# Kernel tuning notes

Hardware: AMD Instinct MI355X
Metric: run time of the kernel (lower is better)

Reference implementation:

```python
import jax, jax.numpy as jnp
import numpy as np

N_NODES = 100000
N_EDGES = 1600000
N_GRAPHS = 512
HIDDEN = 128
N_LAYERS = 3


def setup_inputs() -> dict:
    key = jax.random.key(0)
    ks = jax.random.split(key, 16)
    X = jax.random.normal(ks[0], (N_NODES, HIDDEN), dtype=jnp.float32)
    edge_index = jax.random.randint(ks[1], (2, N_EDGES), 0, N_NODES, dtype=jnp.int64)
    batch = jnp.sort(jax.random.randint(ks[2], (N_NODES,), 0, N_GRAPHS, dtype=jnp.int64))
    s = 1.0 / np.sqrt(HIDDEN)
    mlp_w1 = jax.random.normal(ks[3], (N_LAYERS, HIDDEN, HIDDEN), dtype=jnp.float32) * s
    mlp_b1 = jnp.zeros((N_LAYERS, HIDDEN), dtype=jnp.float32)
    mlp_w2 = jax.random.normal(ks[4], (N_LAYERS, HIDDEN, HIDDEN), dtype=jnp.float32) * s
    mlp_b2 = jnp.zeros((N_LAYERS, HIDDEN), dtype=jnp.float32)
    cls_w1 = jax.random.normal(ks[5], (HIDDEN * N_LAYERS, HIDDEN), dtype=jnp.float32) / np.sqrt(HIDDEN * N_LAYERS)
    cls_b1 = jnp.zeros((HIDDEN,), dtype=jnp.float32)
    cls_w2 = jax.random.normal(ks[6], (HIDDEN, HIDDEN), dtype=jnp.float32) * s
    cls_b2 = jnp.zeros((HIDDEN,), dtype=jnp.float32)
    cls_w3 = jax.random.normal(ks[7], (HIDDEN, 1), dtype=jnp.float32) * s
    cls_b3 = jnp.zeros((1,), dtype=jnp.float32)
    return {"X": X, "edge_index": edge_index, "batch": batch,
            "mlp_w1": mlp_w1, "mlp_b1": mlp_b1, "mlp_w2": mlp_w2, "mlp_b2": mlp_b2,
            "cls_w1": cls_w1, "cls_b1": cls_b1, "cls_w2": cls_w2, "cls_b2": cls_b2,
            "cls_w3": cls_w3, "cls_b3": cls_b3}


def reference(X, edge_index, batch, mlp_w1, mlp_b1, mlp_w2, mlp_b2,
              cls_w1, cls_b1, cls_w2, cls_b2, cls_w3, cls_b3):
    src, dst = edge_index[0], edge_index[1]
    xs = []
    for l in range(N_LAYERS):
        # GIN aggregation: sum_{j in N(i)} x_j ; eps = 0 so add self feature
        agg = jax.ops.segment_sum(X[src], dst, num_segments=N_NODES)  # [N, H]
        z = X + agg
        # 2-layer MLP update
        h = jax.nn.relu(z @ mlp_w1[l] + mlp_b1[l])
        h = h @ mlp_w2[l] + mlp_b2[l]
        # dropout is identity in eval; then relu
        X = jax.nn.relu(h)
        # global sum pooling per graph
        xs.append(jax.ops.segment_sum(X, batch, num_segments=N_GRAPHS))  # [G, H]
    h = jnp.concatenate(xs, axis=-1)  # JK 'cat' -> [G, H*L]
    h = jax.nn.relu(h @ cls_w1 + cls_b1)
    h = jax.nn.relu(h @ cls_w2 + cls_b2)
    logits = h @ cls_w3 + cls_b3  # [G, 1]
    return logits
```

## Files before the change

kernel.cpp:

```cpp
#include <hip/hip_runtime.h>
#include <hip/hip_fp16.h>
#include <cstddef>
#include <cstdint>

#define N_NODES   100000
#define N_EDGES   1600000
#define N_GRAPHS  512
#define HIDDEN    128
#define N_LAYERS  3

#define N_WIN        400
#define WIN_NODES    (N_NODES / N_WIN)
#define PLACE_BLOCKS 128
#define PCHUNK       (N_EDGES / PLACE_BLOCKS)

typedef _Float16 half8  __attribute__((ext_vector_type(8)));
typedef _Float16 half2v __attribute__((ext_vector_type(2)));
typedef float    float8 __attribute__((ext_vector_type(8)));
typedef float    floatx4 __attribute__((ext_vector_type(4)));
typedef float    floatx2 __attribute__((ext_vector_type(2)));

__global__ __launch_bounds__(256) void win_count_kernel(const int* __restrict__ dst,
                                                        int* __restrict__ counts) {
    __shared__ int cs[N_WIN];
    for (int i = threadIdx.x; i < N_WIN; i += 256) cs[i] = 0;
    __syncthreads();
    const int4* d4 = (const int4*)(dst + blockIdx.x * PCHUNK);
    for (int i = threadIdx.x; i < PCHUNK / 4; i += 256) {
        int4 d = d4[i];
        atomicAdd(&cs[d.x / WIN_NODES], 1);
        atomicAdd(&cs[d.y / WIN_NODES], 1);
        atomicAdd(&cs[d.z / WIN_NODES], 1);
        atomicAdd(&cs[d.w / WIN_NODES], 1);
    }
    __syncthreads();
    for (int i = threadIdx.x; i < N_WIN; i += 256)
        counts[blockIdx.x * N_WIN + i] = cs[i];
}

__global__ __launch_bounds__(128) void win_scan1_kernel(const int* __restrict__ counts,
                                                        int* __restrict__ offsets,
                                                        int* __restrict__ colsum) {
    __shared__ int tmp[128];
    const int w = blockIdx.x;
    const int t = threadIdx.x;
    tmp[t] = counts[t * N_WIN + w];
    __syncthreads();
#pragma unroll
    for (int off = 1; off < 128; off <<= 1) {
        int u = (t >= off) ? tmp[t - off] : 0;
        __syncthreads();
        tmp[t] += u;
        __syncthreads();
    }
    offsets[t * N_WIN + w] = (t == 0) ? 0 : tmp[t - 1];
    if (t == 127) colsum[w] = tmp[127];
}

__global__ __launch_bounds__(512) void win_scan2_kernel(const int* __restrict__ colsum,
                                                        int* __restrict__ winbase) {
    __shared__ int tmp[512];
    const int t = threadIdx.x;
    tmp[t] = (t < N_WIN) ? colsum[t] : 0;
    __syncthreads();
#pragma unroll
    for (int off = 1; off < 512; off <<= 1) {
        int u = (t >= off) ? tmp[t - off] : 0;
        __syncthreads();
        tmp[t] += u;
        __syncthreads();
    }
    if (t < N_WIN) winbase[t] = (t == 0) ? 0 : tmp[t - 1];
    if (t == N_WIN - 1) winbase[N_WIN] = tmp[t];
}

__global__ __launch_bounds__(256) void win_place_kernel(const int* __restrict__ src,
                                                        const int* __restrict__ dst,
                                                        const int* __restrict__ offsets,
                                                        const int* __restrict__ winbase,
                                                        int2* __restrict__ wedge) {
    __shared__ int off[N_WIN];
    for (int i = threadIdx.x; i < N_WIN; i += 256)
        off[i] = offsets[blockIdx.x * N_WIN + i] + winbase[i];
    __syncthreads();
    const int4* d4 = (const int4*)(dst + blockIdx.x * PCHUNK);
    const int4* s4 = (const int4*)(src + blockIdx.x * PCHUNK);
    for (int i = threadIdx.x; i < PCHUNK / 4; i += 256) {
        int4 d = d4[i];
        int4 s = s4[i];
        int p0 = atomicAdd(&off[d.x / WIN_NODES], 1); wedge[p0] = make_int2(d.x, s.x);
        int p1 = atomicAdd(&off[d.y / WIN_NODES], 1); wedge[p1] = make_int2(d.y, s.y);
        int p2 = atomicAdd(&off[d.z / WIN_NODES], 1); wedge[p2] = make_int2(d.z, s.z);
        int p3 = atomicAdd(&off[d.w / WIN_NODES], 1); wedge[p3] = make_int2(d.w, s.w);
    }
}

__global__ __launch_bounds__(256) void win_csr_kernel(const int2* __restrict__ wedge,
                                                      const int* __restrict__ winbase,
                                                      int* __restrict__ row_ptr,
                                                      int* __restrict__ csr_src) {
    __shared__ int cnt[WIN_NODES];
    __shared__ int tmp[256];
    const int w = blockIdx.x, n0 = w * WIN_NODES, t = threadIdx.x;
    for (int i = t; i < WIN_NODES; i += 256) cnt[i] = 0;
    __syncthreads();
    const int b0 = winbase[w], b1 = winbase[w + 1];
    for (int e = b0 + t; e < b1; e += 256)
        atomicAdd(&cnt[wedge[e].x - n0], 1);
    __syncthreads();
    tmp[t] = (t < WIN_NODES) ? cnt[t] : 0;
    __syncthreads();
#pragma unroll
    for (int off = 1; off < 256; off <<= 1) {
        int u = (t >= off) ? tmp[t - off] : 0;
        __syncthreads();
        tmp[t] += u;
        __syncthreads();
    }
    const int excl = (t == 0) ? 0 : tmp[t - 1];
    if (t < WIN_NODES) {
        row_ptr[n0 + t] = b0 + excl;
        cnt[t] = b0 + excl;
    }
    if (w == N_WIN - 1 && t == 0) row_ptr[N_NODES] = winbase[N_WIN];
    __syncthreads();
    for (int e = b0 + t; e < b1; e += 256) {
        int2 ed = wedge[e];
        int p = atomicAdd(&cnt[ed.x - n0], 1);
        csr_src[p] = ed.y;
    }
}

__global__ void f2h_kernel(const float* __restrict__ in, __half* __restrict__ out,
                           unsigned char* __restrict__ outq) {
    int t = blockIdx.x * blockDim.x + threadIdx.x;
    const int n8 = (N_NODES * HIDDEN) / 8;
    if (t >= n8) return;
    const float4* in4 = (const float4*)in;
    float4 a = in4[t * 2 + 0];
    float4 b = in4[t * 2 + 1];
    __half2* o2 = (__half2*)out;
    o2[t * 4 + 0] = __floats2half2_rn(a.x, a.y);
    o2[t * 4 + 1] = __floats2half2_rn(a.z, a.w);
    o2[t * 4 + 2] = __floats2half2_rn(b.x, b.y);
    o2[t * 4 + 3] = __floats2half2_rn(b.z, b.w);
    unsigned r0 = 0, r1 = 0;
    r0 = __builtin_amdgcn_cvt_pk_fp8_f32(a.x, a.y, r0, false);
    r0 = __builtin_amdgcn_cvt_pk_fp8_f32(a.z, a.w, r0, true);
    r1 = __builtin_amdgcn_cvt_pk_fp8_f32(b.x, b.y, r1, false);
    r1 = __builtin_amdgcn_cvt_pk_fp8_f32(b.z, b.w, r1, true);
    ((uint2*)outq)[t] = make_uint2(r0, r1);
}

__global__ __launch_bounds__(256) void wconv_kernel(const float* __restrict__ w1,
                                                    const float* __restrict__ w2,
                                                    __half* __restrict__ wt1,
                                                    __half* __restrict__ wt2) {
    __shared__ float tile[32][33];
    const int b = blockIdx.x;
    const int mat = b & 1;
    const int tt = (b >> 1) & 15;
    const int l  = b >> 5;
    const int ti = (tt >> 2) * 32, tj = (tt & 3) * 32;
    const float* W = (mat ? w2 : w1) + (size_t)l * HIDDEN * HIDDEN;
    __half* WT = (mat ? wt2 : wt1) + (size_t)l * HIDDEN * HIDDEN;
    const int r = threadIdx.x >> 5;
    const int c = threadIdx.x & 31;
#pragma unroll
    for (int rr = 0; rr < 4; ++rr)
        tile[r + 8 * rr][c] = W[(size_t)(ti + r + 8 * rr) * HIDDEN + tj + c];
    __syncthreads();
#pragma unroll
    for (int rr = 0; rr < 4; ++rr)
        WT[(size_t)(tj + r + 8 * rr) * HIDDEN + ti + c] =
            __float2half(tile[c][r + 8 * rr]);
}

__device__ __forceinline__ void acc_fp8x16(float* acc, uint4 v) {
    floatx2 f;
    f = __builtin_amdgcn_cvt_pk_f32_fp8(v.x, false); acc[0] += f.x;  acc[1] += f.y;
    f = __builtin_amdgcn_cvt_pk_f32_fp8(v.x, true);  acc[2] += f.x;  acc[3] += f.y;
    f = __builtin_amdgcn_cvt_pk_f32_fp8(v.y, false); acc[4] += f.x;  acc[5] += f.y;
    f = __builtin_amdgcn_cvt_pk_f32_fp8(v.y, true);  acc[6] += f.x;  acc[7] += f.y;
    f = __builtin_amdgcn_cvt_pk_f32_fp8(v.z, false); acc[8] += f.x;  acc[9] += f.y;
    f = __builtin_amdgcn_cvt_pk_f32_fp8(v.z, true);  acc[10] += f.x; acc[11] += f.y;
    f = __builtin_amdgcn_cvt_pk_f32_fp8(v.w, false); acc[12] += f.x; acc[13] += f.y;
    f = __builtin_amdgcn_cvt_pk_f32_fp8(v.w, true);  acc[14] += f.x; acc[15] += f.y;
}

__global__ void gather_kernel(const unsigned char* __restrict__ Xq,
                              const __half* __restrict__ Xh,
                              __half* __restrict__ Zh,
                              const int* __restrict__ row_ptr,
                              const int* __restrict__ csr_src) {
    int wave = (blockIdx.x * blockDim.x + threadIdx.x) >> 6;
    int lane = threadIdx.x & 63;
    if (wave >= N_NODES) return;
    const int grp = lane >> 3;
    const int m   = lane & 7;
    const uint4* Q = (const uint4*)Xq;

    float acc[16];
#pragma unroll
    for (int j = 0; j < 16; ++j) acc[j] = 0.f;

    int k = row_ptr[wave];
    const int end = row_ptr[wave + 1];

    for (; k + 16 <= end; k += 16) {
        int n0 = csr_src[k + grp];
        int n1 = csr_src[k + 8 + grp];
        uint4 v0 = Q[(size_t)n0 * 8 + m];
        uint4 v1 = Q[(size_t)n1 * 8 + m];
        acc_fp8x16(acc, v0);
        acc_fp8x16(acc, v1);
    }
    if (k + 8 <= end) {
        int n0 = csr_src[k + grp];
        uint4 v0 = Q[(size_t)n0 * 8 + m];
        acc_fp8x16(acc, v0);
        k += 8;
    }
    int rem = end - k;
    if (grp < rem) {
        int n0 = csr_src[k + grp];
        uint4 v0 = Q[(size_t)n0 * 8 + m];
        acc_fp8x16(acc, v0);
    }

    half2v hh[8];
#pragma unroll
    for (int j = 0; j < 8; ++j) {
        hh[j][0] = (_Float16)acc[2 * j];
        hh[j][1] = (_Float16)acc[2 * j + 1];
    }
#pragma unroll
    for (int j = 0; j < 8; ++j) {
        int b = __shfl_xor(__builtin_bit_cast(int, hh[j]), 8);
        hh[j] = hh[j] + __builtin_bit_cast(half2v, b);
    }
#pragma unroll
    for (int j = 0; j < 8; ++j) {
        int b = __shfl_xor(__builtin_bit_cast(int, hh[j]), 16);
        hh[j] = hh[j] + __builtin_bit_cast(half2v, b);
    }
#pragma unroll
    for (int j = 0; j < 8; ++j) {
        int b = __shfl_xor(__builtin_bit_cast(int, hh[j]), 32);
        hh[j] = hh[j] + __builtin_bit_cast(half2v, b);
    }

    if (grp == 0) {
        const half2v* H2 = (const half2v*)(Xh + (size_t)wave * HIDDEN + 16 * m);
        half8 o0, o1;
#pragma unroll
        for (int j = 0; j < 4; ++j) {
            half2v s = hh[j] + H2[j];
            o0[2 * j] = s[0]; o0[2 * j + 1] = s[1];
        }
#pragma unroll
        for (int j = 0; j < 4; ++j) {
            half2v s = hh[4 + j] + H2[4 + j];
            o1[2 * j] = s[0]; o1[2 * j + 1] = s[1];
        }
        ((half8*)(Zh + (size_t)wave * HIDDEN + 16 * m))[0] = o0;
        ((half8*)(Zh + (size_t)wave * HIDDEN + 16 * m))[1] = o1;
    }
}

#define MM_BLOCKS 512
__global__ __launch_bounds__(256, 2) void mm_stage_kernel(const __half* __restrict__ A,
                                                          const __half* __restrict__ Wt,
                                                          const float* __restrict__ bias,
                                                          __half* __restrict__ C16) {
    const int gwave = (blockIdx.x * 256 + threadIdx.x) >> 6;
    const int lane  = threadIdx.x & 63;
    const int m = lane & 15;
    const int q = lane >> 4;
    const int nwaves = MM_BLOCKS * 4;
    const int NTILES = N_NODES / 16;

    half8 wf[8][4];
    float bl[8];
#pragma unroll
    for (int ct = 0; ct < 8; ++ct) {
        const half8* Wrow = (const half8*)(Wt + (size_t)(ct * 16 + m) * HIDDEN);
#pragma unroll
        for (int c = 0; c < 4; ++c) wf[ct][c] = Wrow[c * 4 + q];
        bl[ct] = bias[ct * 16 + m];
    }

    for (int t = gwave; t < NTILES; t += nwaves) {
        const half8* Arow = (const half8*)(A + (size_t)(t * 16 + m) * HIDDEN);
        half8 a0 = Arow[q];
        half8 a1 = Arow[4 + q];
        half8 a2 = Arow[8 + q];
        half8 a3 = Arow[12 + q];
#pragma unroll
        for (int ct = 0; ct < 8; ++ct) {
            floatx4 acc = {0.f, 0.f, 0.f, 0.f};
            acc = __builtin_amdgcn_mfma_f32_16x16x32_f16(a0, wf[ct][0], acc, 0, 0, 0);
            acc = __builtin_amdgcn_mfma_f32_16x16x32_f16(a1, wf[ct][1], acc, 0, 0, 0);
            acc = __builtin_amdgcn_mfma_f32_16x16x32_f16(a2, wf[ct][2], acc, 0, 0, 0);
            acc = __builtin_amdgcn_mfma_f32_16x16x32_f16(a3, wf[ct][3], acc, 0, 0, 0);
            const int n = ct * 16 + m;
#pragma unroll
            for (int r = 0; r < 4; ++r) {
                int row = t * 16 + q * 4 + r;
                float v = fmaxf(acc[r] + bl[ct], 0.f);
                C16[(size_t)row * HIDDEN + n] = __float2half(v);
            }
        }
    }
}

#define POOL_CHUNK 32
__global__ __launch_bounds__(64) void pool_kernel(const __half* __restrict__ Xh,
                                                  const int* __restrict__ batch,
                                                  float* __restrict__ pooled, int layer,
                                                  unsigned char* __restrict__ outq) {
    const int f2 = threadIdx.x;
    int start = blockIdx.x * POOL_CHUNK;
    int end = start + POOL_CHUNK;
    if (end > N_NODES) end = N_NODES;
    float ax = 0.f, ay = 0.f;
    int gcur = batch[start];
    for (int n = start; n < end; ++n) {
        int g = batch[n];
        if (g != gcur) {
            float* pd = &pooled[(size_t)gcur * (HIDDEN * N_LAYERS) + layer * HIDDEN + 2 * f2];
            atomicAdd(pd, ax);
            atomicAdd(pd + 1, ay);
            ax = 0.f; ay = 0.f;
            gcur = g;
        }
        __half2 v = ((const __half2*)(Xh + (size_t)n * HIDDEN))[f2];
        float2 fv = __half22float2(v);
        ax += fv.x; ay += fv.y;
        if (outq) {
            unsigned r = __builtin_amdgcn_cvt_pk_fp8_f32(fv.x, fv.y, 0, false);
            ((unsigned short*)(outq + (size_t)n * HIDDEN))[f2] = (unsigned short)(r & 0xffff);
        }
    }
    float* pd = &pooled[(size_t)gcur * (HIDDEN * N_LAYERS) + layer * HIDDEN + 2 * f2];
    atomicAdd(pd, ax);
    atomicAdd(pd + 1, ay);
}

__global__ __launch_bounds__(128) void cls_kernel(const float* __restrict__ pooled,
                                                  const float* __restrict__ w1,
                                                  const float* __restrict__ b1,
                                                  const float* __restrict__ w2,
                                                  const float* __restrict__ b2,
                                                  const float* __restrict__ w3,
                                                  const float* __restrict__ b3,
                                                  float* __restrict__ out) {
    __shared__ float hin[HIDDEN * N_LAYERS];
    __shared__ float h1[HIDDEN];
    __shared__ float red[HIDDEN];
    const int g = blockIdx.x;
    const int t = threadIdx.x;

    for (int i = t; i < HIDDEN * N_LAYERS; i += 128)
        hin[i] = pooled[(size_t)g * (HIDDEN * N_LAYERS) + i];
    __syncthreads();

    float s = 0.f;
    for (int k = 0; k < HIDDEN * N_LAYERS; ++k) s += hin[k] * w1[(size_t)k * HIDDEN + t];
    s = fmaxf(s + b1[t], 0.f);
    h1[t] = s;
    __syncthreads();

    float s2 = 0.f;
    for (int k = 0; k < HIDDEN; ++k) s2 += h1[k] * w2[(size_t)k * HIDDEN + t];
    s2 = fmaxf(s2 + b2[t], 0.f);

    red[t] = s2 * w3[t];
    __syncthreads();
    for (int off = 64; off > 0; off >>= 1) {
        if (t < off) red[t] += red[t + off];
        __syncthreads();
    }
    if (t == 0) out[g] = red[0] + b3[0];
}

extern "C" void kernel_launch(void* const* d_in, const int* in_sizes, int n_in,
                              void* d_out, int out_size, void* d_ws, size_t ws_size,
                              hipStream_t stream) {
    const float* X     = (const float*)d_in[0];
    const int*   ei    = (const int*)d_in[1];
    const int*   batch = (const int*)d_in[2];
    const float* w1all = (const float*)d_in[3];
    const float* b1all = (const float*)d_in[4];
    const float* w2all = (const float*)d_in[5];
    const float* b2all = (const float*)d_in[6];
    const float* cw1   = (const float*)d_in[7];
    const float* cb1   = (const float*)d_in[8];
    const float* cw2   = (const float*)d_in[9];
    const float* cb2   = (const float*)d_in[10];
    const float* cw3   = (const float*)d_in[11];
    const float* cb3   = (const float*)d_in[12];
    float* out = (float*)d_out;

    const int* src = ei;
    const int* dst = ei + N_EDGES;

    char* p = (char*)d_ws;
    auto alloc2 = [&](size_t bytes) {
        char* r = p;
        p += (bytes + 255) & ~(size_t)255;
        return r;
    };
    __half* hA      = (__half*)alloc2((size_t)N_NODES * HIDDEN * sizeof(__half));
    __half* hB      = (__half*)alloc2((size_t)N_NODES * HIDDEN * sizeof(__half));
    __half* zh      = (__half*)alloc2((size_t)N_NODES * HIDDEN * sizeof(__half));
    __half* m1h     = (__half*)alloc2((size_t)N_NODES * HIDDEN * sizeof(__half));
    unsigned char* qbuf = (unsigned char*)alloc2((size_t)N_NODES * HIDDEN);
    __half* wt1     = (__half*)alloc2((size_t)N_LAYERS * HIDDEN * HIDDEN * sizeof(__half));
    __half* wt2     = (__half*)alloc2((size_t)N_LAYERS * HIDDEN * HIDDEN * sizeof(__half));
    int2*   wedge   = (int2*)alloc2((size_t)N_EDGES * sizeof(int2));
    int*    csr     = (int*)alloc2((size_t)N_EDGES * sizeof(int));
    int*    rowp    = (int*)alloc2((size_t)(N_NODES + 1) * sizeof(int));
    int*    counts  = (int*)alloc2((size_t)PLACE_BLOCKS * N_WIN * sizeof(int));
    int*    offsets = (int*)alloc2((size_t)PLACE_BLOCKS * N_WIN * sizeof(int));
    int*    colsum  = (int*)alloc2((size_t)N_WIN * sizeof(int));
    int*    winbase = (int*)alloc2((size_t)(N_WIN + 1) * sizeof(int));
    float*  pooled  = (float*)alloc2((size_t)N_GRAPHS * HIDDEN * N_LAYERS * sizeof(float));

    hipMemsetAsync(pooled, 0, (size_t)N_GRAPHS * HIDDEN * N_LAYERS * sizeof(float), stream);

    win_count_kernel<<<PLACE_BLOCKS, 256, 0, stream>>>(dst, counts);
    win_scan1_kernel<<<N_WIN, 128, 0, stream>>>(counts, offsets, colsum);
    win_scan2_kernel<<<1, 512, 0, stream>>>(colsum, winbase);
    win_place_kernel<<<PLACE_BLOCKS, 256, 0, stream>>>(src, dst, offsets, winbase, wedge);
    win_csr_kernel<<<N_WIN, 256, 0, stream>>>(wedge, winbase, rowp, csr);

    const int cvt_grid = ((N_NODES * HIDDEN / 8) + 255) / 256;
    f2h_kernel<<<cvt_grid, 256, 0, stream>>>(X, hA, qbuf);
    wconv_kernel<<<N_LAYERS * 2 * 16, 256, 0, stream>>>(w1all, w2all, wt1, wt2);

    const int gat_grid  = (N_NODES + 3) / 4;
    const int pool_grid = (N_NODES + POOL_CHUNK - 1) / POOL_CHUNK;

    __half* hcur = hA;
    for (int l = 0; l < N_LAYERS; ++l) {
        __half* hnext = (l & 1) ? hA : hB;
        gather_kernel<<<gat_grid, 256, 0, stream>>>(qbuf, hcur, zh, rowp, csr);
        mm_stage_kernel<<<MM_BLOCKS, 256, 0, stream>>>(zh,
                                                       wt1 + (size_t)l * HIDDEN * HIDDEN,
                                                       b1all + (size_t)l * HIDDEN,
                                                       m1h);
        mm_stage_kernel<<<MM_BLOCKS, 256, 0, stream>>>(m1h,
                                                       wt2 + (size_t)l * HIDDEN * HIDDEN,
                                                       b2all + (size_t)l * HIDDEN,
                                                       hnext);
        pool_kernel<<<pool_grid, 64, 0, stream>>>(hnext, batch, pooled, l,
                                                  (l < N_LAYERS - 1) ? qbuf : nullptr);
        hcur = hnext;
    }

    cls_kernel<<<N_GRAPHS, 128, 0, stream>>>(pooled, cw1, cb1, cw2, cb2, cw3, cb3, out);
}
```

Measured before the change: 487.5 us.

## Fuse setup kernels, inline window scan, and vectorize MFMA output stores

Removes the single-block window scan kernel by having each place and CSR block redundantly recompute the 400-entry prefix sum in shared memory. It also merges the fp16/fp8 input conversion, weight transpose and pooled-buffer zeroing into one prep kernel, which replaces a memset and two launches. Separately, the MLP matmul swaps its MFMA operands so each lane holds four consecutive output columns and writes them with one 8-byte store instead of four scattered 2-byte stores. The cost is redundant scan work in every block and larger 512-thread blocks for the graph-building kernels.

```diff
diff --git a/kernel.cpp b/kernel.cpp
--- a/kernel.cpp
+++ b/kernel.cpp
@@ -14,7 +14,13 @@
 #define PLACE_BLOCKS 128
 #define PCHUNK       (N_EDGES / PLACE_BLOCKS)
 
+#define F2H_BLOCKS   ((N_NODES * HIDDEN / 8) / 256)
+#define WCONV_BLOCKS (N_LAYERS * 2 * 16)
+#define PZERO_BLOCKS ((N_GRAPHS * HIDDEN * N_LAYERS) / 256)
+#define PREP_BLOCKS  (F2H_BLOCKS + WCONV_BLOCKS + PZERO_BLOCKS)
+
 typedef _Float16 half8  __attribute__((ext_vector_type(8)));
+typedef _Float16 half4v __attribute__((ext_vector_type(4)));
 typedef _Float16 half2v __attribute__((ext_vector_type(2)));
 typedef float    float8 __attribute__((ext_vector_type(8)));
 typedef float    floatx4 __attribute__((ext_vector_type(4)));
@@ -57,35 +63,28 @@
     if (t == 127) colsum[w] = tmp[127];
 }
 
-__global__ __launch_bounds__(512) void win_scan2_kernel(const int* __restrict__ colsum,
-                                                        int* __restrict__ winbase) {
-    __shared__ int tmp[512];
-    const int t = threadIdx.x;
-    tmp[t] = (t < N_WIN) ? colsum[t] : 0;
-    __syncthreads();
-#pragma unroll
-    for (int off = 1; off < 512; off <<= 1) {
-        int u = (t >= off) ? tmp[t - off] : 0;
-        __syncthreads();
-        tmp[t] += u;
-        __syncthreads();
-    }
-    if (t < N_WIN) winbase[t] = (t == 0) ? 0 : tmp[t - 1];
-    if (t == N_WIN - 1) winbase[N_WIN] = tmp[t];
-}
-
-__global__ __launch_bounds__(256) void win_place_kernel(const int* __restrict__ src,
+__global__ __launch_bounds__(512) void win_place_kernel(const int* __restrict__ src,
                                                         const int* __restrict__ dst,
                                                         const int* __restrict__ offsets,
-                                                        const int* __restrict__ winbase,
+                                                        const int* __restrict__ colsum,
                                                         int2* __restrict__ wedge) {
+    __shared__ int ws[512];
     __shared__ int off[N_WIN];
-    for (int i = threadIdx.x; i < N_WIN; i += 256)
-        off[i] = offsets[blockIdx.x * N_WIN + i] + winbase[i];
+    const int t = threadIdx.x;
+    ws[t] = (t < N_WIN) ? colsum[t] : 0;
+    __syncthreads();
+#pragma unroll
+    for (int o = 1; o < 512; o <<= 1) {
+        int u = (t >= o) ? ws[t - o] : 0;
+        __syncthreads();
+        ws[t] += u;
+        __syncthreads();
+    }
+    if (t < N_WIN) off[t] = offsets[blockIdx.x * N_WIN + t] + ((t == 0) ? 0 : ws[t - 1]);
     __syncthreads();
     const int4* d4 = (const int4*)(dst + blockIdx.x * PCHUNK);
     const int4* s4 = (const int4*)(src + blockIdx.x * PCHUNK);
-    for (int i = threadIdx.x; i < PCHUNK / 4; i += 256) {
+    for (int i = t; i < PCHUNK / 4; i += 512) {
         int4 d = d4[i];
         int4 s = s4[i];
         int p0 = atomicAdd(&off[d.x / WIN_NODES], 1); wedge[p0] = make_int2(d.x, s.x);
@@ -95,85 +94,101 @@
     }
 }
 
-__global__ __launch_bounds__(256) void win_csr_kernel(const int2* __restrict__ wedge,
-                                                      const int* __restrict__ winbase,
+__global__ __launch_bounds__(512) void win_csr_kernel(const int2* __restrict__ wedge,
+                                                      const int* __restrict__ colsum,
                                                       int* __restrict__ row_ptr,
                                                       int* __restrict__ csr_src) {
+    __shared__ int ws[512];
     __shared__ int cnt[WIN_NODES];
-    __shared__ int tmp[256];
+    __shared__ int bb[2];
     const int w = blockIdx.x, n0 = w * WIN_NODES, t = threadIdx.x;
-    for (int i = t; i < WIN_NODES; i += 256) cnt[i] = 0;
-    __syncthreads();
-    const int b0 = winbase[w], b1 = winbase[w + 1];
-    for (int e = b0 + t; e < b1; e += 256)
+    ws[t] = (t < N_WIN) ? colsum[t] : 0;
+    __syncthreads();
+#pragma unroll
+    for (int o = 1; o < 512; o <<= 1) {
+        int u = (t >= o) ? ws[t - o] : 0;
+        __syncthreads();
+        ws[t] += u;
+        __syncthreads();
+    }
+    if (t == 0) { bb[0] = (w > 0) ? ws[w - 1] : 0; bb[1] = ws[w]; }
+    if (w == N_WIN - 1 && t == 0) row_ptr[N_NODES] = ws[N_WIN - 1];
+    for (int i = t; i < WIN_NODES; i += 512) cnt[i] = 0;
+    __syncthreads();
+    const int b0 = bb[0], b1 = bb[1];
+    for (int e = b0 + t; e < b1; e += 512)
         atomicAdd(&cnt[wedge[e].x - n0], 1);
     __syncthreads();
-    tmp[t] = (t < WIN_NODES) ? cnt[t] : 0;
-    __syncthreads();
-#pragma unroll
-    for (int off = 1; off < 256; off <<= 1) {
-        int u = (t >= off) ? tmp[t - off] : 0;
-        __syncthreads();
-        tmp[t] += u;
-        __syncthreads();
-    }
-    const int excl = (t == 0) ? 0 : tmp[t - 1];
+    ws[t] = (t < WIN_NODES) ? cnt[t] : 0;
+    __syncthreads();
+#pragma unroll
+    for (int o = 1; o < 512; o <<= 1) {
+        int u = (t >= o) ? ws[t - o] : 0;
+        __syncthreads();
+        ws[t] += u;
+        __syncthreads();
+    }
+    const int excl = (t == 0) ? 0 : ws[t - 1];
     if (t < WIN_NODES) {
         row_ptr[n0 + t] = b0 + excl;
         cnt[t] = b0 + excl;
     }
-    if (w == N_WIN - 1 && t == 0) row_ptr[N_NODES] = winbase[N_WIN];
-    __syncthreads();
-    for (int e = b0 + t; e < b1; e += 256) {
+    __syncthreads();
+    for (int e = b0 + t; e < b1; e += 512) {
         int2 ed = wedge[e];
         int p = atomicAdd(&cnt[ed.x - n0], 1);
         csr_src[p] = ed.y;
     }
 }
 
-__global__ void f2h_kernel(const float* __restrict__ in, __half* __restrict__ out,
-                           unsigned char* __restrict__ outq) {
-    int t = blockIdx.x * blockDim.x + threadIdx.x;
-    const int n8 = (N_NODES * HIDDEN) / 8;
-    if (t >= n8) return;
-    const float4* in4 = (const float4*)in;
-    float4 a = in4[t * 2 + 0];
-    float4 b = in4[t * 2 + 1];
-    __half2* o2 = (__half2*)out;
-    o2[t * 4 + 0] = __floats2half2_rn(a.x, a.y);
-    o2[t * 4 + 1] = __floats2half2_rn(a.z, a.w);
-    o2[t * 4 + 2] = __floats2half2_rn(b.x, b.y);
-    o2[t * 4 + 3] = __floats2half2_rn(b.z, b.w);
-    unsigned r0 = 0, r1 = 0;
-    r0 = __builtin_amdgcn_cvt_pk_fp8_f32(a.x, a.y, r0, false);
-    r0 = __builtin_amdgcn_cvt_pk_fp8_f32(a.z, a.w, r0, true);
-    r1 = __builtin_amdgcn_cvt_pk_fp8_f32(b.x, b.y, r1, false);
-    r1 = __builtin_amdgcn_cvt_pk_fp8_f32(b.z, b.w, r1, true);
-    ((uint2*)outq)[t] = make_uint2(r0, r1);
-}
-
-__global__ __launch_bounds__(256) void wconv_kernel(const float* __restrict__ w1,
-                                                    const float* __restrict__ w2,
-                                                    __half* __restrict__ wt1,
-                                                    __half* __restrict__ wt2) {
+__global__ __launch_bounds__(256) void prep_kernel(const float* __restrict__ X,
+                                                   __half* __restrict__ hA,
+                                                   unsigned char* __restrict__ outq,
+                                                   const float* __restrict__ w1,
+                                                   const float* __restrict__ w2,
+                                                   __half* __restrict__ wt1,
+                                                   __half* __restrict__ wt2,
+                                                   float* __restrict__ pooled) {
     __shared__ float tile[32][33];
     const int b = blockIdx.x;
-    const int mat = b & 1;
-    const int tt = (b >> 1) & 15;
-    const int l  = b >> 5;
-    const int ti = (tt >> 2) * 32, tj = (tt & 3) * 32;
-    const float* W = (mat ? w2 : w1) + (size_t)l * HIDDEN * HIDDEN;
-    __half* WT = (mat ? wt2 : wt1) + (size_t)l * HIDDEN * HIDDEN;
-    const int r = threadIdx.x >> 5;
-    const int c = threadIdx.x & 31;
-#pragma unroll
-    for (int rr = 0; rr < 4; ++rr)
-        tile[r + 8 * rr][c] = W[(size_t)(ti + r + 8 * rr) * HIDDEN + tj + c];
-    __syncthreads();
-#pragma unroll
-    for (int rr = 0; rr < 4; ++rr)
-        WT[(size_t)(tj + r + 8 * rr) * HIDDEN + ti + c] =
-            __float2half(tile[c][r + 8 * rr]);
+    if (b < F2H_BLOCKS) {
+        int t = b * 256 + threadIdx.x;
+        const float4* in4 = (const float4*)X;
+        float4 a = in4[t * 2 + 0];
+        float4 c = in4[t * 2 + 1];
+        __half2* o2 = (__half2*)hA;
+        o2[t * 4 + 0] = __floats2half2_rn(a.x, a.y);
+        o2[t * 4 + 1] = __floats2half2_rn(a.z, a.w);
+        o2[t * 4 + 2] = __floats2half2_rn(c.x, c.y);
+        o2[t * 4 + 3] = __floats2half2_rn(c.z, c.w);
+        unsigned r0 = 0, r1 = 0;
+        r0 = __builtin_amdgcn_cvt_pk_fp8_f32(a.x, a.y, r0, false);
+        r0 = __builtin_amdgcn_cvt_pk_fp8_f32(a.z, a.w, r0, true);
+        r1 = __builtin_amdgcn_cvt_pk_fp8_f32(c.x, c.y, r1, false);
+        r1 = __builtin_amdgcn_cvt_pk_fp8_f32(c.z, c.w, r1, true);
+        ((uint2*)outq)[t] = make_uint2(r0, r1);
+    } else if (b < F2H_BLOCKS + WCONV_BLOCKS) {
+        const int bb = b - F2H_BLOCKS;
+        const int mat = bb & 1;
+        const int tt = (bb >> 1) & 15;
+        const int l  = bb >> 5;
+        const int ti = (tt >> 2) * 32, tj = (tt & 3) * 32;
+        const float* W = (mat ? w2 : w1) + (size_t)l * HIDDEN * HIDDEN;
+        __half* WT = (mat ? wt2 : wt1) + (size_t)l * HIDDEN * HIDDEN;
+        const int r = threadIdx.x >> 5;
+        const int c = threadIdx.x & 31;
+#pragma unroll
+        for (int rr = 0; rr < 4; ++rr)
+            tile[r + 8 * rr][c] = W[(size_t)(ti + r + 8 * rr) * HIDDEN + tj + c];
+        __syncthreads();
+#pragma unroll
+        for (int rr = 0; rr < 4; ++rr)
+            WT[(size_t)(tj + r + 8 * rr) * HIDDEN + ti + c] =
+                __float2half(tile[c][r + 8 * rr]);
+    } else {
+        int idx = (b - F2H_BLOCKS - WCONV_BLOCKS) * 256 + threadIdx.x;
+        pooled[idx] = 0.f;
+    }
 }
 
 __device__ __forceinline__ void acc_fp8x16(float* acc, uint4 v) {
@@ -281,13 +296,14 @@
     const int NTILES = N_NODES / 16;
 
     half8 wf[8][4];
-    float bl[8];
+    float bl[8][4];
 #pragma unroll
     for (int ct = 0; ct < 8; ++ct) {
         const half8* Wrow = (const half8*)(Wt + (size_t)(ct * 16 + m) * HIDDEN);
 #pragma unroll
         for (int c = 0; c < 4; ++c) wf[ct][c] = Wrow[c * 4 + q];
-        bl[ct] = bias[ct * 16 + m];
+#pragma unroll
+        for (int r = 0; r < 4; ++r) bl[ct][r] = bias[ct * 16 + q * 4 + r];
     }
 
     for (int t = gwave; t < NTILES; t += nwaves) {
@@ -296,20 +312,19 @@
         half8 a1 = Arow[4 + q];
         half8 a2 = Arow[8 + q];
         half8 a3 = Arow[12 + q];
+        __half* Cr = C16 + (size_t)(t * 16 + m) * HIDDEN + q * 4;
 #pragma unroll
         for (int ct = 0; ct < 8; ++ct) {
             floatx4 acc = {0.f, 0.f, 0.f, 0.f};
-            acc = __builtin_amdgcn_mfma_f32_16x16x32_f16(a0, wf[ct][0], acc, 0, 0, 0);
-            acc = __builtin_amdgcn_mfma_f32_16x16x32_f16(a1, wf[ct][1], acc, 0, 0, 0);
-            acc = __builtin_amdgcn_mfma_f32_16x16x32_f16(a2, wf[ct][2], acc, 0, 0, 0);
-            acc = __builtin_amdgcn_mfma_f32_16x16x32_f16(a3, wf[ct][3], acc, 0, 0, 0);
-            const int n = ct * 16 + m;
-#pragma unroll
-            for (int r = 0; r < 4; ++r) {
-                int row = t * 16 + q * 4 + r;
-                float v = fmaxf(acc[r] + bl[ct], 0.f);
-                C16[(size_t)row * HIDDEN + n] = __float2half(v);
-            }
+            acc = __builtin_amdgcn_mfma_f32_16x16x32_f16(wf[ct][0], a0, acc, 0, 0, 0);
+            acc = __builtin_amdgcn_mfma_f32_16x16x32_f16(wf[ct][1], a1, acc, 0, 0, 0);
+            acc = __builtin_amdgcn_mfma_f32_16x16x32_f16(wf[ct][2], a2, acc, 0, 0, 0);
+            acc = __builtin_amdgcn_mfma_f32_16x16x32_f16(wf[ct][3], a3, acc, 0, 0, 0);
+            half4v o;
+#pragma unroll
+            for (int r = 0; r < 4; ++r)
+                o[r] = (_Float16)fmaxf(acc[r] + bl[ct][r], 0.f);
+            *(half4v*)(Cr + ct * 16) = o;
         }
     }
 }
@@ -424,20 +439,14 @@
     int*    counts  = (int*)alloc2((size_t)PLACE_BLOCKS * N_WIN * sizeof(int));
     int*    offsets = (int*)alloc2((size_t)PLACE_BLOCKS * N_WIN * sizeof(int));
     int*    colsum  = (int*)alloc2((size_t)N_WIN * sizeof(int));
-    int*    winbase = (int*)alloc2((size_t)(N_WIN + 1) * sizeof(int));
     float*  pooled  = (float*)alloc2((size_t)N_GRAPHS * HIDDEN * N_LAYERS * sizeof(float));
-
-    hipMemsetAsync(pooled, 0, (size_t)N_GRAPHS * HIDDEN * N_LAYERS * sizeof(float), stream);
 
     win_count_kernel<<<PLACE_BLOCKS, 256, 0, stream>>>(dst, counts);
     win_scan1_kernel<<<N_WIN, 128, 0, stream>>>(counts, offsets, colsum);
-    win_scan2_kernel<<<1, 512, 0, stream>>>(colsum, winbase);
-    win_place_kernel<<<PLACE_BLOCKS, 256, 0, stream>>>(src, dst, offsets, winbase, wedge);
-    win_csr_kernel<<<N_WIN, 256, 0, stream>>>(wedge, winbase, rowp, csr);
-
-    const int cvt_grid = ((N_NODES * HIDDEN / 8) + 255) / 256;
-    f2h_kernel<<<cvt_grid, 256, 0, stream>>>(X, hA, qbuf);
-    wconv_kernel<<<N_LAYERS * 2 * 16, 256, 0, stream>>>(w1all, w2all, wt1, wt2);
+    win_place_kernel<<<PLACE_BLOCKS, 512, 0, stream>>>(src, dst, offsets, colsum, wedge);
+    win_csr_kernel<<<N_WIN, 512, 0, stream>>>(wedge, colsum, rowp, csr);
+
+    prep_kernel<<<PREP_BLOCKS, 256, 0, stream>>>(X, hA, qbuf, w1all, w2all, wt1, wt2, pooled);
 
     const int gat_grid  = (N_NODES + 3) / 4;
     const int pool_grid = (N_NODES + POOL_CHUNK - 1) / POOL_CHUNK;
```

New measurement: 478.5 us. About the same (-1.8%).
